# Performance work log

Measured on AMD Instinct MI355X. Metric: run time of the kernel, lower is better.

Reference implementation:

```python
import jax, jax.numpy as jnp
import numpy as np

EMB = 4096
HEADS = 32
SCALE = 4
D = EMB // HEADS          # qkv_dim = 128
HKV = HEADS // SCALE      # 8 kv heads
B, S = 2, 2048


def setup_inputs() -> dict:
    key = jax.random.key(0)
    ks = jax.random.split(key, 7)
    std = 0.02
    return {
        "x": jax.random.normal(ks[0], (B, S, EMB), jnp.float32),
        "Wq": jax.random.normal(ks[1], (EMB, D, HEADS), jnp.float32) * std,
        "bq": jnp.zeros((D, HEADS), jnp.float32),
        "Wk": jax.random.normal(ks[2], (EMB, D, HKV), jnp.float32) * std,
        "bk": jnp.zeros((D, HKV), jnp.float32),
        "Wv": jax.random.normal(ks[3], (EMB, D, HKV), jnp.float32) * std,
        "bv": jnp.zeros((D, HKV), jnp.float32),
    }


def reference(x, Wq, bq, Wk, bk, Wv, bv):
    # DenseGeneral projections: (B,S,E) -> (B,S,D,H)
    q = jnp.einsum("bse,edh->bsdh", x, Wq) + bq          # [B,S,D,H]
    k = jnp.einsum("bse,edh->bsdh", x, Wk) + bk          # [B,S,D,Hkv]
    v = jnp.einsum("bse,edh->bsdh", x, Wv) + bv          # [B,S,D,Hkv]
    # repeat kv heads (each kv head duplicated SCALE times, matching jnp.repeat)
    k = jnp.repeat(k, SCALE, axis=-1)                    # [B,S,D,H]
    v = jnp.repeat(v, SCALE, axis=-1)                    # [B,S,D,H]
    # NOTE: as written in the source, attention contracts the HEAD axis per
    # token: scores are (qkv_dim x qkv_dim) per (b, s) position.
    scores = jnp.einsum("bsdh,bseh->bsde", q, k) / np.float32(np.sqrt(D))
    attn = jax.nn.softmax(scores, axis=-1)               # [B,S,D,D]
    out = jnp.einsum("bsde,bseh->bsdh", attn, v)         # [B,S,D,H]
    return out.reshape(x.shape[:-1] + (EMB,))
```

## Files before the change

kernel.cpp:

```cpp
#include <hip/hip_runtime.h>
#include <cstdint>

typedef unsigned short ushort_t;
typedef __bf16 bf16x8 __attribute__((ext_vector_type(8)));
typedef float f32x4 __attribute__((ext_vector_type(4)));
typedef float f32x2 __attribute__((ext_vector_type(2)));

__device__ __forceinline__ unsigned short f2bf(float f) {
  unsigned u = __builtin_bit_cast(unsigned, f);
  u += 0x7FFFu + ((u >> 16) & 1u);
  return (unsigned short)(u >> 16);
}
__device__ __forceinline__ float bflo(unsigned u) {
  return __builtin_bit_cast(float, u << 16);
}
__device__ __forceinline__ float bfhi(unsigned u) {
  return __builtin_bit_cast(float, u & 0xFFFF0000u);
}
__device__ __forceinline__ void gld16(const void* g, void* l) {
  auto* gp = reinterpret_cast<const __attribute__((address_space(1))) unsigned*>(
      reinterpret_cast<uintptr_t>(g));
  auto* lp = reinterpret_cast<__attribute__((address_space(3))) unsigned*>(
      reinterpret_cast<uintptr_t>(l));
  __builtin_amdgcn_global_load_lds(gp, lp, 16, 0, 0);
}

__global__ __launch_bounds__(256) void prep_all(
    const float* __restrict__ x, const float* __restrict__ Wq,
    const float* __restrict__ Wk, const float* __restrict__ Wv,
    const float* __restrict__ bq, const float* __restrict__ bk,
    const float* __restrict__ bv, ushort_t* __restrict__ Ax,
    ushort_t* __restrict__ Wt, float* __restrict__ bias) {
  __shared__ ushort_t red[64][65];
  const int b = blockIdx.x;
  const int tid = threadIdx.x;
  if (b < 3072) {
    const int ntile = b % 48, ktile = b / 48;
    const int n0 = ntile * 64, k0 = ktile * 64;
    if (ntile < 16) {
      for (int i = tid; i < 64 * 64; i += 256) {
        const int kk = i >> 6, nn = i & 63;
        const float4 w = *reinterpret_cast<const float4*>(
            Wq + (size_t)(k0 + kk) * 4096 + (size_t)(n0 + nn) * 4);
        red[kk][nn] = f2bf(w.x + w.y + w.z + w.w);
      }
    } else {
      const float* W = (ntile < 32) ? Wk : Wv;
      const int nb = (ntile < 32) ? (n0 - 1024) : (n0 - 2048);
      for (int i = tid; i < 64 * 64; i += 256) {
        const int kk = i >> 6, nn = i & 63;
        red[kk][nn] = f2bf(W[(size_t)(k0 + kk) * 1024 + nb + nn]);
      }
    }
    __syncthreads();
    for (int i = tid; i < 64 * 64; i += 256) {
      const int kk = i & 63, nn = i >> 6;
      Wt[(size_t)(n0 + nn) * 4096 + k0 + kk] = red[kk][nn];
    }
  } else if (b < 11264) {
    const size_t i = ((size_t)(b - 3072) * 256 + tid) * 8;
    const float4 a = *reinterpret_cast<const float4*>(x + i);
    const float4 c = *reinterpret_cast<const float4*>(x + i + 4);
    union { ushort_t u[8]; uint4 v; } pk;
    pk.u[0] = f2bf(a.x); pk.u[1] = f2bf(a.y); pk.u[2] = f2bf(a.z); pk.u[3] = f2bf(a.w);
    pk.u[4] = f2bf(c.x); pk.u[5] = f2bf(c.y); pk.u[6] = f2bf(c.z); pk.u[7] = f2bf(c.w);
    *reinterpret_cast<uint4*>(Ax + i) = pk.v;
  } else {
    const int n = (b - 11264) * 256 + tid;
    float v;
    if (n < 1024) {
      const float4 w = *reinterpret_cast<const float4*>(bq + (size_t)n * 4);
      v = w.x + w.y + w.z + w.w;
    } else if (n < 2048) {
      v = bk[n - 1024];
    } else {
      v = bv[n - 2048];
    }
    bias[n] = v;
  }
}

#define WAITV0() asm volatile("s_waitcnt vmcnt(0)" ::: "memory")
#define BARRIER()                         \
  do {                                    \
    __builtin_amdgcn_s_barrier();         \
    asm volatile("" ::: "memory");        \
    __builtin_amdgcn_sched_barrier(0);    \
  } while (0)

__global__ __launch_bounds__(512, 2) void gemm_qkv(const ushort_t* __restrict__ A,
                                                   const ushort_t* __restrict__ Bt,
                                                   const float* __restrict__ bias,
                                                   ushort_t* __restrict__ C) {
  __shared__ char smem[114688];
  ushort_t* AsBuf = reinterpret_cast<ushort_t*>(smem);
  ushort_t* BsBuf = reinterpret_cast<ushort_t*>(smem + 65536);
  const int tid = threadIdx.x;
  const int lane = tid & 63, wave = tid >> 6;

  const int id = blockIdx.x;
  const int wg = (id & 7) * 32 + (id >> 3);
  const int M0 = (wg >> 4) * 256, N0 = (wg & 15) * 192;

  const int rik = lane >> 3;
  const int gch = (lane & 7) ^ rik;
  const ushort_t* aG = A + (size_t)(M0 + wave * 32 + rik) * 4096 + gch * 8;
  const ushort_t* bG = Bt + (size_t)(N0 + wave * 24 + rik) * 4096 + gch * 8;

  const int kh = wave & 1, wq = wave >> 1;
  const int wm = wq >> 1, wn = wq & 1;
  const int quad = lane >> 4, l15 = lane & 15;

  const int ch = ((kh * 4 + quad) ^ (l15 & 7)) * 16;
  const int abase = (wm * 128 + l15) * 128 + ch;
  const int bbase = (wn * 96 + l15) * 128 + ch;

  f32x4 acc[8][6];
  const f32x4 z = {0.f, 0.f, 0.f, 0.f};
#pragma unroll
  for (int mi = 0; mi < 8; ++mi)
#pragma unroll
    for (int ni = 0; ni < 6; ++ni) acc[mi][ni] = z;

  auto stage = [&](int bb, int kt) {
    const int ko = kt * 64;
    ushort_t* asb = AsBuf + bb * 16384;
    ushort_t* bsb = BsBuf + bb * 12288;
#pragma unroll
    for (int q = 0; q < 4; ++q)
      gld16(aG + ko + (size_t)q * (8 * 4096), asb + (wave * 4 + q) * 512);
#pragma unroll
    for (int q = 0; q < 3; ++q)
      gld16(bG + ko + (size_t)q * (8 * 4096), bsb + (wave * 3 + q) * 512);
  };

  stage(0, 0);
  WAITV0();
  BARRIER();

  for (int kt = 0; kt < 64; ++kt) {
    const int bb = kt & 1;
    if (kt < 63) stage(bb ^ 1, kt + 1);
    const char* ab = reinterpret_cast<const char*>(AsBuf + bb * 16384);
    const char* bbp = reinterpret_cast<const char*>(BsBuf + bb * 12288);
    bf16x8 af[8];
#pragma unroll
    for (int mi = 0; mi < 8; ++mi)
      af[mi] = *reinterpret_cast<const bf16x8*>(ab + abase + mi * 2048);
#pragma unroll
    for (int ni = 0; ni < 6; ++ni) {
      const bf16x8 bf = *reinterpret_cast<const bf16x8*>(bbp + bbase + ni * 2048);
      __builtin_amdgcn_s_setprio(1);
#pragma unroll
      for (int mi = 0; mi < 8; ++mi)
        acc[mi][ni] =
            __builtin_amdgcn_mfma_f32_16x16x32_bf16(af[mi], bf, acc[mi][ni], 0, 0, 0);
      __builtin_amdgcn_s_setprio(0);
    }
    WAITV0();
    BARRIER();
  }

  float* scr = reinterpret_cast<float*>(smem);
  const int slot = (wq * 64 + lane) * 97;
#pragma unroll
  for (int p = 0; p < 2; ++p) {
    __syncthreads();
    if (kh == 1) {
#pragma unroll
      for (int mi = 0; mi < 4; ++mi)
#pragma unroll
        for (int ni = 0; ni < 6; ++ni)
#pragma unroll
          for (int r = 0; r < 4; ++r)
            scr[slot + (mi * 6 + ni) * 4 + r] = acc[p * 4 + mi][ni][r];
    }
    __syncthreads();
    if (kh == 0) {
#pragma unroll
      for (int ni = 0; ni < 6; ++ni) {
        const int cc = N0 + wn * 96 + ni * 16 + l15;
        const float bn = bias[cc];
#pragma unroll
        for (int mi = 0; mi < 4; ++mi) {
          const int gmi = p * 4 + mi;
          const int r0 = M0 + wm * 128 + gmi * 16 + quad * 4;
#pragma unroll
          for (int r = 0; r < 4; ++r)
            C[(size_t)(r0 + r) * 3072 + cc] =
                f2bf(acc[gmi][ni][r] + scr[slot + (mi * 6 + ni) * 4 + r] + bn);
        }
      }
    }
  }
}

__global__ __launch_bounds__(256, 4) void attn_tok(const ushort_t* __restrict__ C,
                                                   float* __restrict__ out) {
  __shared__ uint4 kv4[4][256];
  const int tid = threadIdx.x;
  const int lane = tid & 63, wv = tid >> 6;
  const int t = blockIdx.x * 4 + wv;
  const ushort_t* Crow = C + (size_t)t * 3072;

  const ushort_t* kvg = Crow + 1024;
#pragma unroll
  for (int r = 0; r < 4; ++r)
    gld16(kvg + r * 512 + lane * 8, &kv4[wv][r * 64]);

  const uint4 q01 = *reinterpret_cast<const uint4*>(Crow + lane * 16);
  const uint4 q23 = *reinterpret_cast<const uint4*>(Crow + lane * 16 + 8);
  f32x2 q2[8];
  q2[0] = f32x2{bflo(q01.x), bflo(q23.x)};
  q2[1] = f32x2{bfhi(q01.x), bfhi(q23.x)};
  q2[2] = f32x2{bflo(q01.y), bflo(q23.y)};
  q2[3] = f32x2{bfhi(q01.y), bfhi(q23.y)};
  q2[4] = f32x2{bflo(q01.z), bflo(q23.z)};
  q2[5] = f32x2{bfhi(q01.z), bfhi(q23.z)};
  q2[6] = f32x2{bflo(q01.w), bflo(q23.w)};
  q2[7] = f32x2{bfhi(q01.w), bfhi(q23.w)};

  WAITV0();

  const uint4* kvw = kv4[wv];
  const float sc = 0.08838834764831845f;
  f32x2 o2[8];
#pragma unroll
  for (int j = 0; j < 8; ++j) o2[j] = f32x2{0.f, 0.f};
  f32x2 lsum = f32x2{0.f, 0.f};

#pragma unroll 2
  for (int e = 0; e < 128; ++e) {
    const uint4 kr = kvw[e];
    float kf[8];
    kf[0] = bflo(kr.x); kf[1] = bfhi(kr.x); kf[2] = bflo(kr.y); kf[3] = bfhi(kr.y);
    kf[4] = bflo(kr.z); kf[5] = bfhi(kr.z); kf[6] = bflo(kr.w); kf[7] = bfhi(kr.w);
    f32x2 s = f32x2{0.f, 0.f};
#pragma unroll
    for (int j = 0; j < 8; ++j) s += q2[j] * kf[j];
    const f32x2 p = f32x2{__expf(s.x * sc), __expf(s.y * sc)};
    lsum += p;
    const uint4 vr = kvw[128 + e];
    float vf[8];
    vf[0] = bflo(vr.x); vf[1] = bfhi(vr.x); vf[2] = bflo(vr.y); vf[3] = bfhi(vr.y);
    vf[4] = bflo(vr.z); vf[5] = bfhi(vr.z); vf[6] = bflo(vr.w); vf[7] = bfhi(vr.w);
#pragma unroll
    for (int j = 0; j < 8; ++j) o2[j] += p * vf[j];
  }

  const float i0 = 1.f / lsum.x, i1 = 1.f / lsum.y;
  float4* dst = reinterpret_cast<float4*>(out + (size_t)t * 4096 + (size_t)lane * 64);
#pragma unroll
  for (int j = 0; j < 8; ++j) {
    const float w = o2[j].x * i0;
    dst[j] = make_float4(w, w, w, w);
  }
#pragma unroll
  for (int j = 0; j < 8; ++j) {
    const float w = o2[j].y * i1;
    dst[8 + j] = make_float4(w, w, w, w);
  }
}

extern "C" void kernel_launch(void* const* d_in, const int* in_sizes, int n_in,
                              void* d_out, int out_size, void* d_ws, size_t ws_size,
                              hipStream_t stream) {
  const float* x  = (const float*)d_in[0];
  const float* Wq = (const float*)d_in[1];
  const float* bq = (const float*)d_in[2];
  const float* Wk = (const float*)d_in[3];
  const float* bk = (const float*)d_in[4];
  const float* Wv = (const float*)d_in[5];
  const float* bv = (const float*)d_in[6];
  float* out = (float*)d_out;

  ushort_t* Ax = (ushort_t*)d_out;
  ushort_t* Wt = Ax + (size_t)4096 * 4096;
  float* bias = (float*)(Wt + (size_t)3072 * 4096);
  ushort_t* Cmat = (ushort_t*)d_ws;

  prep_all<<<dim3(11276), 256, 0, stream>>>(x, Wq, Wk, Wv, bq, bk, bv, Ax, Wt, bias);
  gemm_qkv<<<dim3(256), 512, 0, stream>>>(Ax, Wt, bias, Cmat);
  attn_tok<<<dim3(1024), 256, 0, stream>>>(Cmat, out);
}
```

Measured before the change: 345.9 us.

## Load B tile directly from global into registers, bypassing LDS

The B operand no longer goes through shared memory. Each wave loads its own B fragments straight from global memory into registers, double-buffered across two register sets, while A stays staged in LDS via global_load_lds. The main loop is unrolled by two to alternate the buffers. This removes the B LDS writes and reads and shrinks LDS use, but it adds register pressure and duplicated global reads of B across the wm waves, with uncoalesced 16-byte strided loads.

Result: slower. 613.9 us (+77.5%).

```diff
diff --git a/kernel.cpp b/kernel.cpp
--- a/kernel.cpp
+++ b/kernel.cpp
@@ -92,9 +92,8 @@
                                                    const ushort_t* __restrict__ Bt,
                                                    const float* __restrict__ bias,
                                                    ushort_t* __restrict__ C) {
-  __shared__ char smem[114688];
+  __shared__ char smem[99328];
   ushort_t* AsBuf = reinterpret_cast<ushort_t*>(smem);
-  ushort_t* BsBuf = reinterpret_cast<ushort_t*>(smem + 65536);
   const int tid = threadIdx.x;
   const int lane = tid & 63, wave = tid >> 6;
 
@@ -105,7 +104,6 @@
   const int rik = lane >> 3;
   const int gch = (lane & 7) ^ rik;
   const ushort_t* aG = A + (size_t)(M0 + wave * 32 + rik) * 4096 + gch * 8;
-  const ushort_t* bG = Bt + (size_t)(N0 + wave * 24 + rik) * 4096 + gch * 8;
 
   const int kh = wave & 1, wq = wave >> 1;
   const int wm = wq >> 1, wn = wq & 1;
@@ -113,7 +111,8 @@
 
   const int ch = ((kh * 4 + quad) ^ (l15 & 7)) * 16;
   const int abase = (wm * 128 + l15) * 128 + ch;
-  const int bbase = (wn * 96 + l15) * 128 + ch;
+
+  const ushort_t* bD = Bt + (size_t)(N0 + wn * 96 + l15) * 4096 + kh * 32 + quad * 8;
 
   f32x4 acc[8][6];
   const f32x4 z = {0.f, 0.f, 0.f, 0.f};
@@ -125,38 +124,50 @@
   auto stage = [&](int bb, int kt) {
     const int ko = kt * 64;
     ushort_t* asb = AsBuf + bb * 16384;
-    ushort_t* bsb = BsBuf + bb * 12288;
 #pragma unroll
     for (int q = 0; q < 4; ++q)
       gld16(aG + ko + (size_t)q * (8 * 4096), asb + (wave * 4 + q) * 512);
-#pragma unroll
-    for (int q = 0; q < 3; ++q)
-      gld16(bG + ko + (size_t)q * (8 * 4096), bsb + (wave * 3 + q) * 512);
   };
-
+  auto loadB = [&](bf16x8* dst, int kt) {
+    const ushort_t* p = bD + kt * 64;
+#pragma unroll
+    for (int ni = 0; ni < 6; ++ni)
+      dst[ni] = *reinterpret_cast<const bf16x8*>(p + ni * (16 * 4096));
+  };
+  auto compute = [&](int bb, const bf16x8* bfr) {
+    const char* ab = reinterpret_cast<const char*>(AsBuf + bb * 16384);
+    bf16x8 af[8];
+#pragma unroll
+    for (int mi = 0; mi < 8; ++mi)
+      af[mi] = *reinterpret_cast<const bf16x8*>(ab + abase + mi * 2048);
+#pragma unroll
+    for (int ni = 0; ni < 6; ++ni) {
+      __builtin_amdgcn_s_setprio(1);
+#pragma unroll
+      for (int mi = 0; mi < 8; ++mi)
+        acc[mi][ni] =
+            __builtin_amdgcn_mfma_f32_16x16x32_bf16(af[mi], bfr[ni], acc[mi][ni], 0, 0, 0);
+      __builtin_amdgcn_s_setprio(0);
+    }
+  };
+
+  bf16x8 bA[6], bB[6];
   stage(0, 0);
+  loadB(bA, 0);
   WAITV0();
   BARRIER();
 
-  for (int kt = 0; kt < 64; ++kt) {
-    const int bb = kt & 1;
-    if (kt < 63) stage(bb ^ 1, kt + 1);
-    const char* ab = reinterpret_cast<const char*>(AsBuf + bb * 16384);
-    const char* bbp = reinterpret_cast<const char*>(BsBuf + bb * 12288);
-    bf16x8 af[8];
-#pragma unroll
-    for (int mi = 0; mi < 8; ++mi)
-      af[mi] = *reinterpret_cast<const bf16x8*>(ab + abase + mi * 2048);
-#pragma unroll
-    for (int ni = 0; ni < 6; ++ni) {
-      const bf16x8 bf = *reinterpret_cast<const bf16x8*>(bbp + bbase + ni * 2048);
-      __builtin_amdgcn_s_setprio(1);
-#pragma unroll
-      for (int mi = 0; mi < 8; ++mi)
-        acc[mi][ni] =
-            __builtin_amdgcn_mfma_f32_16x16x32_bf16(af[mi], bf, acc[mi][ni], 0, 0, 0);
-      __builtin_amdgcn_s_setprio(0);
-    }
+  for (int t = 0; t < 64; t += 2) {
+    stage(1, t + 1);
+    loadB(bB, t + 1);
+    compute(0, bA);
+    WAITV0();
+    BARRIER();
+    if (t + 2 < 64) {
+      stage(0, t + 2);
+      loadB(bA, t + 2);
+    }
+    compute(1, bB);
     WAITV0();
     BARRIER();
   }
```
